# Performance work log

Measured on AMD Instinct MI355X. Metric: run time of the kernel, lower is better.

Reference implementation:

```python
import jax, jax.numpy as jnp
import numpy as np


def _multinomial_sample(t, gumbel, k):
    # t: [R, S] non-negative weights (R = batch*hidden). Torch's
    # torch.multinomial(t, k) (without replacement) is distributionally
    # equivalent to top-k of log(t) + Gumbel noise (Gumbel top-k trick).
    row_sum = jnp.sum(t, axis=1, keepdims=True)          # [R, 1]
    mask = (row_sum == 0).astype(t.dtype)                # [R, 1]
    t = t + mask                                         # zero rows -> uniform
    scores = jnp.log(t) + gumbel                         # log(0) = -inf: never picked
    _, idx = jax.lax.top_k(scores, k)                    # [R, k] sampled w/o replacement
    vals = jnp.take_along_axis(t, idx, axis=1)           # gather sampled weights
    vals = vals + mask * (-1.0)                          # undo the +1 on masked rows
    return vals.sum(axis=1)                              # [R]


def setup_inputs() -> dict:
    key = jax.random.key(0)
    k1, k2, k3, k4 = jax.random.split(key, 4)
    B, S, H = 8, 4096, 1024
    hidden_states = jax.random.normal(k1, (B, S, H), dtype=jnp.float32)
    u = jax.random.uniform(k2, (B * H, S), dtype=jnp.float32, minval=1e-6, maxval=1.0)
    gumbel = -jnp.log(-jnp.log(u))
    W = jax.random.normal(k3, (H, H), dtype=jnp.float32) * 0.02
    b = jax.random.normal(k4, (H,), dtype=jnp.float32) * 0.02
    return {"hidden_states": hidden_states, "gumbel": gumbel, "W": W, "b": b, "sample": 8}


def reference(hidden_states, gumbel, W, b, sample):
    B, S, H = hidden_states.shape
    rep = jax.nn.relu(hidden_states)                     # [B, S, H]
    t = rep.transpose(0, 2, 1).reshape(-1, S)            # [B*H, S]
    pooled = _multinomial_sample(t, gumbel, sample).reshape(B, H)
    out = pooled @ W.T + b                               # nn.Linear(H, H)
    return jnp.tanh(out)
```

## Files before the change

### kernel.cpp

```cpp
#include <hip/hip_runtime.h>
#include <math.h>

#define BB 8
#define SS 4096
#define HH 1024
#define ROWS (BB * HH)
#define KTOP 8
#define NS 32
#define SC (SS / NS)
#define SCW (SC / 4)
#define NB (SCW / 8)

#define INSERT8(TS, TV, SCV, VALV) do {                                   \
    if ((SCV) > TS[7]) {                                                  \
      TS[7] = (SCV); TV[7] = (VALV);                                      \
      _Pragma("unroll")                                                   \
      for (int _i = 7; _i > 0; --_i) {                                    \
        if (TS[_i] > TS[_i - 1]) {                                        \
          float _t = TS[_i]; TS[_i] = TS[_i - 1]; TS[_i - 1] = _t;        \
          float _v = TV[_i]; TV[_i] = TV[_i - 1]; TV[_i - 1] = _v;        \
        }                                                                 \
      }                                                                   \
    }                                                                     \
  } while (0)

__global__ __launch_bounds__(256) void topk_partial(
    const float* __restrict__ hidden, const float* __restrict__ gumbel,
    float2* __restrict__ pairs) {
  __shared__ float2 lst[256 * 9];

  const int tid = threadIdx.x;
  const int rl  = tid & 63;
  const int w   = tid >> 6;
  const int sc  = blockIdx.x;
  const int rb  = blockIdx.y;
  const int r   = rb * 64 + rl;
  const int b   = rb >> 4;
  const int h0  = (rb & 15) << 6;
  const int s_base = sc * SC + w * SCW;

  const float* __restrict__ hcol = hidden + ((size_t)b * SS) * HH + h0 + rl;
  const float4* __restrict__ gp =
      (const float4*)(gumbel + (size_t)r * SS + s_base);

  float ts[KTOP], tv[KTOP];
#pragma unroll
  for (int i = 0; i < KTOP; ++i) { ts[i] = -INFINITY; tv[i] = 0.0f; }

  float4 ga = gp[0], gb = gp[1];
  float hb[8];
  {
    const float* __restrict__ hp = hcol + (size_t)s_base * HH;
#pragma unroll
    for (int i = 0; i < 8; ++i) hb[i] = hp[(size_t)i * HH];
  }
#pragma unroll
  for (int k = 0; k < NB; ++k) {
    float4 gna, gnb; float hn[8];
    if (k + 1 < NB) {
      gna = gp[2 * k + 2]; gnb = gp[2 * k + 3];
      const float* __restrict__ hp = hcol + (size_t)(s_base + 8 * (k + 1)) * HH;
#pragma unroll
      for (int i = 0; i < 8; ++i) hn[i] = hp[(size_t)i * HH];
    }
    const float g[8] = {ga.x, ga.y, ga.z, ga.w, gb.x, gb.y, gb.z, gb.w};
#pragma unroll
    for (int i = 0; i < 8; ++i) {
      const float t   = fmaxf(hb[i], 0.0f);
      const float scv = logf(t) + g[i];
      INSERT8(ts, tv, scv, t);
    }
    if (k + 1 < NB) {
      ga = gna; gb = gnb;
#pragma unroll
      for (int i = 0; i < 8; ++i) hb[i] = hn[i];
    }
  }

#pragma unroll
  for (int j = 0; j < KTOP; ++j)
    lst[(w * 64 + rl) * 9 + j] = make_float2(ts[j], tv[j]);
  __syncthreads();
  if (w == 0 || w == 2) {
#pragma unroll
    for (int j = 0; j < KTOP; ++j) {
      const float2 p = lst[((w + 1) * 64 + rl) * 9 + j];
      INSERT8(ts, tv, p.x, p.y);
    }
    if (w == 2) {
#pragma unroll
      for (int j = 0; j < KTOP; ++j)
        lst[(2 * 64 + rl) * 9 + j] = make_float2(ts[j], tv[j]);
    }
  }
  __syncthreads();
  if (w == 0) {
#pragma unroll
    for (int j = 0; j < KTOP; ++j) {
      const float2 p = lst[(2 * 64 + rl) * 9 + j];
      INSERT8(ts, tv, p.x, p.y);
    }
    float2* __restrict__ op = pairs + ((size_t)r * NS + sc) * KTOP;
#pragma unroll
    for (int j = 0; j < KTOP; ++j) op[j] = make_float2(ts[j], tv[j]);
  }
}

__global__ __launch_bounds__(256) void topk_merge(
    const float2* __restrict__ pairs, float* __restrict__ pooled) {
  __shared__ float2 ls[256 * 9];
  const int tid  = threadIdx.x;
  const int rloc = tid >> 3;
  const int q    = tid & 7;
  const int r    = blockIdx.x * 32 + rloc;
  const int slot = rloc * 8 + q;

  float ts[KTOP], tv[KTOP];
#pragma unroll
  for (int i = 0; i < KTOP; ++i) { ts[i] = -INFINITY; tv[i] = 0.0f; }

  const int cpg = NS / 8;
  const float4* __restrict__ p =
      (const float4*)(pairs + ((size_t)r * NS + q * cpg) * KTOP);
#pragma unroll
  for (int i = 0; i < cpg * KTOP / 2; ++i) {
    const float4 two = p[i];
    INSERT8(ts, tv, two.x, two.y);
    INSERT8(ts, tv, two.z, two.w);
  }
#pragma unroll
  for (int j = 0; j < KTOP; ++j) ls[slot * 9 + j] = make_float2(ts[j], tv[j]);
  __syncthreads();
  if ((q & 1) == 0) {
#pragma unroll
    for (int j = 0; j < KTOP; ++j) {
      const float2 pp = ls[(slot + 1) * 9 + j];
      INSERT8(ts, tv, pp.x, pp.y);
    }
#pragma unroll
    for (int j = 0; j < KTOP; ++j) ls[slot * 9 + j] = make_float2(ts[j], tv[j]);
  }
  __syncthreads();
  if ((q & 3) == 0) {
#pragma unroll
    for (int j = 0; j < KTOP; ++j) {
      const float2 pp = ls[(slot + 2) * 9 + j];
      INSERT8(ts, tv, pp.x, pp.y);
    }
#pragma unroll
    for (int j = 0; j < KTOP; ++j) ls[slot * 9 + j] = make_float2(ts[j], tv[j]);
  }
  __syncthreads();
  if (q == 0) {
#pragma unroll
    for (int j = 0; j < KTOP; ++j) {
      const float2 pp = ls[(slot + 4) * 9 + j];
      INSERT8(ts, tv, pp.x, pp.y);
    }
    float sum = 0.0f;
#pragma unroll
    for (int j = 0; j < KTOP; ++j) sum += tv[j];
    pooled[r] = sum;
  }
}

__global__ __launch_bounds__(256) void linear_tanh(
    const float* __restrict__ pooled, const float* __restrict__ W,
    const float* __restrict__ bias, float* __restrict__ out) {
  __shared__ float lp[ROWS];
  const int tid = threadIdx.x;
#pragma unroll
  for (int i = 0; i < ROWS / 4 / 256; ++i)
    ((float4*)lp)[i * 256 + tid] = ((const float4*)pooled)[i * 256 + tid];
  __syncthreads();

  const int wave = tid >> 6;
  const int lane = tid & 63;
  const int j = blockIdx.x * 4 + wave;

  float acc[BB];
#pragma unroll
  for (int bb = 0; bb < BB; ++bb) acc[bb] = 0.0f;
#pragma unroll
  for (int k0 = 0; k0 < HH; k0 += 256) {
    const float4 w4 = *(const float4*)&W[(size_t)j * HH + k0 + lane * 4];
#pragma unroll
    for (int bb = 0; bb < BB; ++bb) {
      const float4 p4 = *(const float4*)&lp[bb * HH + k0 + lane * 4];
      acc[bb] += w4.x * p4.x + w4.y * p4.y + w4.z * p4.z + w4.w * p4.w;
    }
  }
#pragma unroll
  for (int bb = 0; bb < BB; ++bb) {
    float a = acc[bb];
    for (int off = 32; off > 0; off >>= 1) a += __shfl_down(a, off, 64);
    if (lane == 0) out[(size_t)bb * HH + j] = tanhf(a + bias[j]);
  }
}

extern "C" void kernel_launch(void* const* d_in, const int* in_sizes, int n_in,
                              void* d_out, int out_size, void* d_ws, size_t ws_size,
                              hipStream_t stream) {
  const float* hidden = (const float*)d_in[0];
  const float* gumbel = (const float*)d_in[1];
  const float* W      = (const float*)d_in[2];
  const float* bias   = (const float*)d_in[3];
  float* out          = (float*)d_out;

  float2* pairs  = (float2*)d_ws;
  float*  pooled = (float*)((char*)d_ws
                   + (size_t)ROWS * NS * KTOP * sizeof(float2));

  topk_partial<<<dim3(NS, ROWS / 64), dim3(256), 0, stream>>>(hidden, gumbel, pairs);
  topk_merge<<<dim3(ROWS / 32), dim3(256), 0, stream>>>(pairs, pooled);
  linear_tanh<<<dim3(HH / 4), dim3(256), 0, stream>>>(pooled, W, bias, out);
}
```

Measured before the change: 321.1 us.

## Stage hidden tiles through LDS with coalesced float4 loads, one row per thread

The partial top-k kernel now gives each thread a whole row over its sequence chunk, so the cross-wave merge is gone. Hidden tiles are loaded with coalesced float4 reads into a double-buffered LDS tile. The score log(t)+g is replaced by the monotone-equivalent t*exp(g), and the initial sentinel becomes -1 so zero-weight entries can still be kept. This cuts strided scalar global loads and the log calls, at the cost of a __syncthreads per tile, fewer blocks, and a changed order (and so tie and rounding behaviour) for ranking sampled entries.

Measured after the change: 326.2 us. No clear change (+1.6%).

```diff
diff --git a/kernel.cpp b/kernel.cpp
--- a/kernel.cpp
+++ b/kernel.cpp
@@ -8,17 +8,17 @@
 #define KTOP 8
 #define NS 32
 #define SC (SS / NS)
-#define SCW (SC / 4)
-#define NB (SCW / 8)
-
-#define INSERT8(TS, TV, SCV, VALV) do {                                   \
-    if ((SCV) > TS[7]) {                                                  \
-      TS[7] = (SCV); TV[7] = (VALV);                                      \
+#define TS 8
+#define NT (SC / TS)
+
+#define INSERT8(TS_, TV_, SCV, VALV) do {                                 \
+    if ((SCV) > TS_[7]) {                                                 \
+      TS_[7] = (SCV); TV_[7] = (VALV);                                    \
       _Pragma("unroll")                                                   \
       for (int _i = 7; _i > 0; --_i) {                                    \
-        if (TS[_i] > TS[_i - 1]) {                                        \
-          float _t = TS[_i]; TS[_i] = TS[_i - 1]; TS[_i - 1] = _t;        \
-          float _v = TV[_i]; TV[_i] = TV[_i - 1]; TV[_i - 1] = _v;        \
+        if (TS_[_i] > TS_[_i - 1]) {                                      \
+          float _t = TS_[_i]; TS_[_i] = TS_[_i - 1]; TS_[_i - 1] = _t;    \
+          float _v = TV_[_i]; TV_[_i] = TV_[_i - 1]; TV_[_i - 1] = _v;    \
         }                                                                 \
       }                                                                   \
     }                                                                     \
@@ -27,83 +27,66 @@
 __global__ __launch_bounds__(256) void topk_partial(
     const float* __restrict__ hidden, const float* __restrict__ gumbel,
     float2* __restrict__ pairs) {
-  __shared__ float2 lst[256 * 9];
+  __shared__ float lh[2][TS * 256];
 
   const int tid = threadIdx.x;
-  const int rl  = tid & 63;
-  const int w   = tid >> 6;
   const int sc  = blockIdx.x;
   const int rb  = blockIdx.y;
-  const int r   = rb * 64 + rl;
-  const int b   = rb >> 4;
-  const int h0  = (rb & 15) << 6;
-  const int s_base = sc * SC + w * SCW;
-
-  const float* __restrict__ hcol = hidden + ((size_t)b * SS) * HH + h0 + rl;
+  const int r   = rb * 256 + tid;
+  const int b   = rb >> 2;
+  const int h0  = (rb & 3) << 8;
+  const int s0  = sc * SC;
+
+  const float* __restrict__ hbase = hidden + (size_t)b * SS * HH + h0;
   const float4* __restrict__ gp =
-      (const float4*)(gumbel + (size_t)r * SS + s_base);
+      (const float4*)(gumbel + (size_t)r * SS + s0);
+
+  const int sil = tid >> 6;
+  const int hq  = tid & 63;
 
   float ts[KTOP], tv[KTOP];
 #pragma unroll
-  for (int i = 0; i < KTOP; ++i) { ts[i] = -INFINITY; tv[i] = 0.0f; }
-
-  float4 ga = gp[0], gb = gp[1];
-  float hb[8];
+  for (int i = 0; i < KTOP; ++i) { ts[i] = -1.0f; tv[i] = 0.0f; }
+
   {
-    const float* __restrict__ hp = hcol + (size_t)s_base * HH;
-#pragma unroll
-    for (int i = 0; i < 8; ++i) hb[i] = hp[(size_t)i * HH];
-  }
-#pragma unroll
-  for (int k = 0; k < NB; ++k) {
-    float4 gna, gnb; float hn[8];
-    if (k + 1 < NB) {
-      gna = gp[2 * k + 2]; gnb = gp[2 * k + 3];
-      const float* __restrict__ hp = hcol + (size_t)(s_base + 8 * (k + 1)) * HH;
-#pragma unroll
-      for (int i = 0; i < 8; ++i) hn[i] = hp[(size_t)i * HH];
-    }
-    const float g[8] = {ga.x, ga.y, ga.z, ga.w, gb.x, gb.y, gb.z, gb.w};
-#pragma unroll
-    for (int i = 0; i < 8; ++i) {
-      const float t   = fmaxf(hb[i], 0.0f);
-      const float scv = logf(t) + g[i];
-      INSERT8(ts, tv, scv, t);
-    }
-    if (k + 1 < NB) {
-      ga = gna; gb = gnb;
-#pragma unroll
-      for (int i = 0; i < 8; ++i) hb[i] = hn[i];
-    }
-  }
-
-#pragma unroll
-  for (int j = 0; j < KTOP; ++j)
-    lst[(w * 64 + rl) * 9 + j] = make_float2(ts[j], tv[j]);
-  __syncthreads();
-  if (w == 0 || w == 2) {
-#pragma unroll
-    for (int j = 0; j < KTOP; ++j) {
-      const float2 p = lst[((w + 1) * 64 + rl) * 9 + j];
-      INSERT8(ts, tv, p.x, p.y);
-    }
-    if (w == 2) {
-#pragma unroll
-      for (int j = 0; j < KTOP; ++j)
-        lst[(2 * 64 + rl) * 9 + j] = make_float2(ts[j], tv[j]);
-    }
-  }
-  __syncthreads();
-  if (w == 0) {
-#pragma unroll
-    for (int j = 0; j < KTOP; ++j) {
-      const float2 p = lst[(2 * 64 + rl) * 9 + j];
-      INSERT8(ts, tv, p.x, p.y);
-    }
-    float2* __restrict__ op = pairs + ((size_t)r * NS + sc) * KTOP;
-#pragma unroll
-    for (int j = 0; j < KTOP; ++j) op[j] = make_float2(ts[j], tv[j]);
-  }
+#pragma unroll
+    for (int p = 0; p < 2; ++p) {
+      const int si = p * 4 + sil;
+      const float4 v = *(const float4*)&hbase[(size_t)(s0 + si) * HH + hq * 4];
+      *(float4*)&lh[0][si * 256 + hq * 4] = v;
+    }
+  }
+  float4 g0 = gp[0], g1 = gp[1];
+  __syncthreads();
+
+  for (int t = 0; t < NT; ++t) {
+    const int cur = t & 1;
+    float4 nh0, nh1, ng0, ng1;
+    if (t + 1 < NT) {
+      const int sb = s0 + (t + 1) * TS;
+      nh0 = *(const float4*)&hbase[(size_t)(sb + sil) * HH + hq * 4];
+      nh1 = *(const float4*)&hbase[(size_t)(sb + 4 + sil) * HH + hq * 4];
+      ng0 = gp[2 * (t + 1)];
+      ng1 = gp[2 * (t + 1) + 1];
+    }
+    const float g[8] = {g0.x, g0.y, g0.z, g0.w, g1.x, g1.y, g1.z, g1.w};
+#pragma unroll
+    for (int si = 0; si < TS; ++si) {
+      const float tt  = fmaxf(lh[cur][si * 256 + tid], 0.0f);
+      const float key = tt * __expf(g[si]);
+      INSERT8(ts, tv, key, tt);
+    }
+    if (t + 1 < NT) {
+      *(float4*)&lh[cur ^ 1][(sil) * 256 + hq * 4]     = nh0;
+      *(float4*)&lh[cur ^ 1][(4 + sil) * 256 + hq * 4] = nh1;
+      g0 = ng0; g1 = ng1;
+    }
+    __syncthreads();
+  }
+
+  float2* __restrict__ op = pairs + ((size_t)r * NS + sc) * KTOP;
+#pragma unroll
+  for (int j = 0; j < KTOP; ++j) op[j] = make_float2(ts[j], tv[j]);
 }
 
 __global__ __launch_bounds__(256) void topk_merge(
@@ -211,7 +194,7 @@
   float*  pooled = (float*)((char*)d_ws
                    + (size_t)ROWS * NS * KTOP * sizeof(float2));
 
-  topk_partial<<<dim3(NS, ROWS / 64), dim3(256), 0, stream>>>(hidden, gumbel, pairs);
+  topk_partial<<<dim3(NS, 32), dim3(256), 0, stream>>>(hidden, gumbel, pairs);
   topk_merge<<<dim3(ROWS / 32), dim3(256), 0, stream>>>(pairs, pooled);
   linear_tanh<<<dim3(HH / 4), dim3(256), 0, stream>>>(pooled, W, bias, out);
 }
```
